# Kernel tuning notes

Measured on AMD Instinct MI355X. Metric: run time of the kernel, lower is better.

The kernel has to match this reference:

```python
import jax, jax.numpy as jnp
import numpy as np

B, C, H, W = 4, 64, 64, 64  # batch, channels (in==out), spatial


def _conv1x1(x, w, b):
    # x: (B, C, H, W), w: (O, C), b: (O,) -> (B, O, H, W)
    return jnp.einsum('bchw,oc->bohw', x, w) + b[None, :, None, None]


def setup_inputs() -> dict:
    key = jax.random.key(0)
    ks = jax.random.split(key, 7)
    s = 1.0 / np.sqrt(C)
    return {
        'x': jax.random.normal(ks[0], (B, C, H, W), dtype=jnp.float32),
        'Wq': jax.random.normal(ks[1], (C, C), dtype=jnp.float32) * s,
        'bq': jax.random.normal(ks[2], (C,), dtype=jnp.float32) * 0.01,
        'Wk': jax.random.normal(ks[3], (C, C), dtype=jnp.float32) * s,
        'bk': jax.random.normal(ks[4], (C,), dtype=jnp.float32) * 0.01,
        'Wv': jax.random.normal(ks[5], (C, C), dtype=jnp.float32) * s,
        'bv': jax.random.normal(ks[6], (C,), dtype=jnp.float32) * 0.01,
    }


def reference(x, Wq, bq, Wk, bk, Wv, bv):
    b, c, h, w = x.shape
    n = h * w  # number of spatial tokens
    q = _conv1x1(x, Wq, bq).reshape(b, c, n)  # (B, C, N)
    k = _conv1x1(x, Wk, bk).reshape(b, c, n)  # (B, C, N)
    v = _conv1x1(x, Wv, bv).reshape(b, c, n)  # (B, C, N)
    # attention[b, i, j] = softmax_j( q[:, i] . k[:, j] )  -- NOTE: no 1/sqrt(d) scaling, faithful to source
    scores = jnp.einsum('bci,bcj->bij', q, k)  # (B, N, N)
    attn = jax.nn.softmax(scores, axis=-1)
    # out = bmm(value, attention^T): out[b, c, i] = sum_j v[b, c, j] * attn[b, i, j]
    out = jnp.einsum('bcj,bij->bci', v, attn)
    return out.reshape(b, c, h, w)
```

## Files before the change

kernel.cpp:

```cpp
#include <hip/hip_runtime.h>
#include <hip/hip_bf16.h>


using f16    = _Float16;
using f16x8  = __attribute__((ext_vector_type(8))) f16;
using f32x16 = __attribute__((ext_vector_type(16))) float;
using i32x4  = __attribute__((ext_vector_type(4))) int;

static constexpr int NB = 4;
static constexpr int NC = 64;
static constexpr int NT = 4096;
static constexpr int KVB = 64;
static constexpr float LOG2E = 1.44269504088896f;

__device__ __forceinline__ float fexp2(float x) { return __builtin_amdgcn_exp2f(x); }
__device__ __forceinline__ unsigned int pkrtz(float a, float b) {
    return __builtin_bit_cast(unsigned int, __builtin_amdgcn_cvt_pkrtz(a, b));
}

__global__ __launch_bounds__(256) void qkv_proj(
    const float* __restrict__ x,
    const float* __restrict__ Wq, const float* __restrict__ bq,
    const float* __restrict__ Wk, const float* __restrict__ bk,
    const float* __restrict__ Wv, const float* __restrict__ bv,
    f16* __restrict__ qh, f16* __restrict__ kh, f16* __restrict__ vv)
{
    __shared__ f16 xT[64 * 64];
    __shared__ f16 wS[64 * 64];

    const int t  = threadIdx.x;
    const int p  = blockIdx.x >> 8;
    const int b  = (blockIdx.x >> 6) & 3;
    const int n0 = (blockIdx.x & 63) << 6;

    const float* Wp = (p == 0) ? Wq : (p == 1) ? Wk : Wv;
    const float* bp = (p == 0) ? bq : (p == 1) ? bk : bv;

    char* const xb = (char*)xT;
    char* const wb = (char*)wS;

    #pragma unroll
    for (int i = 0; i < 4; ++i) {
        const int idx = i * 256 + t;
        const int c = idx >> 4, n4 = (idx & 15) << 2;
        const float4 xv = *reinterpret_cast<const float4*>(
            x + ((size_t)(b * NC + c)) * NT + n0 + n4);
        const float xe[4] = {xv.x, xv.y, xv.z, xv.w};
        #pragma unroll
        for (int j = 0; j < 4; ++j) {
            const int n = n4 + j;
            *reinterpret_cast<f16*>(xb + n * 128 + ((c * 2) ^ ((n & 7) << 4))) =
                (f16)xe[j];
        }
        const int o = idx >> 4, c4 = (idx & 15) << 2;
        const float4 wv4 = *reinterpret_cast<const float4*>(Wp + o * 64 + c4);
        const uint2 pk = make_uint2(pkrtz(wv4.x, wv4.y), pkrtz(wv4.z, wv4.w));
        *reinterpret_cast<uint2*>(wb + o * 128 + ((c4 * 2) ^ ((o & 7) << 4))) = pk;
    }
    __syncthreads();

    const int lane = t & 63;
    const int wv   = t >> 6;
    const int l31  = lane & 31;
    const int hi   = lane >> 5;
    const int tr   = (wv & 1) << 5;
    const int tc   = (wv >> 1) << 5;

    f32x16 acc = {0,0,0,0,0,0,0,0,0,0,0,0,0,0,0,0};

    if (p < 2) {
        const int ra = tr + l31, rb = tc + l31;
        #pragma unroll
        for (int ks = 0; ks < 4; ++ks) {
            const int col = ks * 32 + hi * 16;
            const f16x8 a = *reinterpret_cast<const f16x8*>(
                xb + ra * 128 + (col ^ ((ra & 7) << 4)));
            const f16x8 bf = *reinterpret_cast<const f16x8*>(
                wb + rb * 128 + (col ^ ((rb & 7) << 4)));
            acc = __builtin_amdgcn_mfma_f32_32x32x16_f16(a, bf, acc, 0, 0, 0);
        }
        f16* hp = (p == 0) ? qh : kh;
        const float qs = (p == 0) ? LOG2E : 1.0f;
        const float bias = bp[tc + l31];
        #pragma unroll
        for (int r = 0; r < 16; ++r) {
            const int row = (r & 3) + 8 * (r >> 2) + 4 * hi;
            hp[((size_t)(b * NT + n0 + tr + row)) * NC + tc + l31] =
                (f16)((acc[r] + bias) * qs);
        }
    } else {
        const int ra = tr + l31, rb = tc + l31;
        #pragma unroll
        for (int ks = 0; ks < 4; ++ks) {
            const int col = ks * 32 + hi * 16;
            const f16x8 a = *reinterpret_cast<const f16x8*>(
                wb + ra * 128 + (col ^ ((ra & 7) << 4)));
            const f16x8 bf = *reinterpret_cast<const f16x8*>(
                xb + rb * 128 + (col ^ ((rb & 7) << 4)));
            acc = __builtin_amdgcn_mfma_f32_32x32x16_f16(a, bf, acc, 0, 0, 0);
        }
        #pragma unroll
        for (int r = 0; r < 16; ++r) {
            const int row = (r & 3) + 8 * (r >> 2) + 4 * hi;
            vv[((size_t)(b * NC + tr + row)) * NT + n0 + tc + l31] =
                (f16)(acc[r] + bp[tr + row]);
        }
    }
}

__global__ __launch_bounds__(256, 4) void attn_fused(
    const f16* __restrict__ qh, const f16* __restrict__ kh,
    const f16* __restrict__ vv, float* __restrict__ out,
    f16* __restrict__ pacc, float* __restrict__ pm,
    float* __restrict__ pl, int nTiles, int direct)
{
    __shared__ f16 khs[KVB * 64];
    __shared__ f16 vs_[64 * KVB];

    const int t    = threadIdx.x;
    const int lane = t & 63;
    const int wv   = t >> 6;
    const int l31  = lane & 31;
    const int hi   = lane >> 5;

    const int ngrp = (int)gridDim.x >> 5;
    int grp, i0;
    if ((ngrp & 7) == 0) {
        const int gpx  = ngrp >> 3;
        const int slot = (int)blockIdx.x >> 3;
        grp = ((int)blockIdx.x & 7) * gpx + (slot >> 5);
        i0  = (slot & 31) << 7;
    } else {
        grp = (int)blockIdx.x >> 5;
        i0  = ((int)blockIdx.x & 31) << 7;
    }
    const int s = grp >> 2;
    const int b = grp & 3;

    f16x8 qf[4];
    {
        const size_t qoff = ((size_t)(b * NT + i0 + wv * 32 + l31)) * NC + hi * 8;
        #pragma unroll
        for (int ks = 0; ks < 4; ++ks)
            qf[ks] = *reinterpret_cast<const f16x8*>(qh + qoff + ks * 16);
    }

    f32x16 acc0 = {0,0,0,0,0,0,0,0,0,0,0,0,0,0,0,0};
    f32x16 acc1 = {0,0,0,0,0,0,0,0,0,0,0,0,0,0,0,0};
    float m = -INFINITY, l = 0.f;

    const int row0 = t >> 3, c8 = (t & 7) << 3;
    const f16* kh_g = kh + (size_t)b * NT * NC;
    const f16* v_g  = vv + (size_t)b * NC * NT;

    char* const khsb = (char*)khs;
    char* const vsb  = (char*)vs_;
    const int kw0 = row0 * 128 + ((c8 << 1) ^ ((row0 & 7) << 4));
    const int kw1 = (row0 + 32) * 128 + ((c8 << 1) ^ (((row0 + 32) & 7) << 4));

    f16x8 stK0, stK1, stV0, stV1;
    auto stage_load = [&](int j0) {
        stK0 = *reinterpret_cast<const f16x8*>(kh_g + (size_t)(j0 + row0) * NC + c8);
        stK1 = *reinterpret_cast<const f16x8*>(kh_g + (size_t)(j0 + row0 + 32) * NC + c8);
        stV0 = *reinterpret_cast<const f16x8*>(v_g + (size_t)row0 * NT + j0 + c8);
        stV1 = *reinterpret_cast<const f16x8*>(v_g + (size_t)(row0 + 32) * NT + j0 + c8);
    };

    const int t0 = s * nTiles;
    stage_load(t0 * KVB);

    for (int k = 0; k < nTiles; ++k) {
        __syncthreads();
        *reinterpret_cast<f16x8*>(khsb + kw0) = stK0;
        *reinterpret_cast<f16x8*>(khsb + kw1) = stK1;
        *reinterpret_cast<f16x8*>(vsb + kw0)  = stV0;
        *reinterpret_cast<f16x8*>(vsb + kw1)  = stV1;
        __syncthreads();
        if (k + 1 < nTiles) stage_load((t0 + k + 1) * KVB);

        f32x16 sS0 = {0,0,0,0,0,0,0,0,0,0,0,0,0,0,0,0};
        f32x16 sS1 = {0,0,0,0,0,0,0,0,0,0,0,0,0,0,0,0};
        #pragma unroll
        for (int ks = 0; ks < 4; ++ks) {
            const int col = ks * 32 + hi * 16;
            const int r0 = l31;
            const f16x8 ak0 = *reinterpret_cast<const f16x8*>(
                khsb + r0 * 128 + (col ^ ((r0 & 7) << 4)));
            sS0 = __builtin_amdgcn_mfma_f32_32x32x16_f16(ak0, qf[ks], sS0, 0, 0, 0);
            const int r1 = 32 + l31;
            const f16x8 ak1 = *reinterpret_cast<const f16x8*>(
                khsb + r1 * 128 + (col ^ ((r1 & 7) << 4)));
            sS1 = __builtin_amdgcn_mfma_f32_32x32x16_f16(ak1, qf[ks], sS1, 0, 0, 0);
        }

        float mx[8];
        #pragma unroll
        for (int i = 0; i < 8; ++i)
            mx[i] = fmaxf(fmaxf(sS0[i], sS0[i + 8]), fmaxf(sS1[i], sS1[i + 8]));
        #pragma unroll
        for (int i = 0; i < 4; ++i) mx[i] = fmaxf(mx[i], mx[i + 4]);
        mx[0] = fmaxf(mx[0], mx[2]); mx[1] = fmaxf(mx[1], mx[3]);
        float mt = fmaxf(mx[0], mx[1]);
        mt = fmaxf(mt, __shfl_xor(mt, 32));
        const float mn = fmaxf(m, mt);

        float rs = 0.f;
        #pragma unroll
        for (int r = 0; r < 16; ++r) { sS0[r] = fexp2(sS0[r] - mn); rs += sS0[r]; }
        #pragma unroll
        for (int r = 0; r < 16; ++r) { sS1[r] = fexp2(sS1[r] - mn); rs += sS1[r]; }
        rs += __shfl_xor(rs, 32);

        if (__any(mt > m)) {
            const float sc = fexp2(m - mn);
            m = mn;
            l = l * sc + rs;
            #pragma unroll
            for (int r = 0; r < 16; ++r) { acc0[r] *= sc; acc1[r] *= sc; }
        } else {
            l += rs;
        }

        auto pv_sub = [&](const f32x16& sX, int kb) {
            unsigned int aw[4], bw[4];
            #pragma unroll
            for (int q4 = 0; q4 < 4; ++q4) {
                aw[q4] = pkrtz(sX[q4 * 4 + 0], sX[q4 * 4 + 1]);
                bw[q4] = pkrtz(sX[q4 * 4 + 2], sX[q4 * 4 + 3]);
            }
            #pragma unroll
            for (int ks = 0; ks < 2; ++ks) {
                const unsigned int ua = hi ? aw[2 * ks] : aw[2 * ks + 1];
                const unsigned int ub = hi ? bw[2 * ks] : bw[2 * ks + 1];
                const unsigned int sa = (unsigned int)__shfl_xor((int)ua, 32);
                const unsigned int sb = (unsigned int)__shfl_xor((int)ub, 32);
                const unsigned int w0 = hi ? sa : aw[2 * ks];
                const unsigned int w1 = hi ? sb : bw[2 * ks];
                const unsigned int w2 = hi ? aw[2 * ks + 1] : sa;
                const unsigned int w3 = hi ? bw[2 * ks + 1] : sb;
                const i32x4 wv4 = {(int)w0, (int)w1, (int)w2, (int)w3};
                const f16x8 bf = __builtin_bit_cast(f16x8, wv4);

                const int vcol = kb * 64 + ks * 32 + hi * 16;
                const int vrow0 = l31;
                const f16x8 av0 = *reinterpret_cast<const f16x8*>(
                    vsb + vrow0 * 128 + (vcol ^ ((vrow0 & 7) << 4)));
                acc0 = __builtin_amdgcn_mfma_f32_32x32x16_f16(av0, bf, acc0, 0, 0, 0);
                const int vrow1 = 32 + l31;
                const f16x8 av1 = *reinterpret_cast<const f16x8*>(
                    vsb + vrow1 * 128 + (vcol ^ ((vrow1 & 7) << 4)));
                acc1 = __builtin_amdgcn_mfma_f32_32x32x16_f16(av1, bf, acc1, 0, 0, 0);
            }
        };
        pv_sub(sS0, 0);
        pv_sub(sS1, 1);
    }

    const int q = i0 + wv * 32 + l31;
    const float linv = 1.f / l;
    if (direct) {
        const size_t ob = (size_t)b * NC * NT;
        #pragma unroll
        for (int r = 0; r < 16; ++r) {
            const int ch = (r & 3) + 8 * (r >> 2) + 4 * hi;
            out[ob + (size_t)ch * NT + q]        = acc0[r] * linv;
            out[ob + (size_t)(32 + ch) * NT + q] = acc1[r] * linv;
        }
    } else {
        const size_t pb = (size_t)(s * NB + b);
        #pragma unroll
        for (int r = 0; r < 16; ++r) {
            const int ch = (r & 3) + 8 * (r >> 2) + 4 * hi;
            pacc[(pb * NC + ch) * NT + q]      = (f16)(acc0[r] * linv);
            pacc[(pb * NC + 32 + ch) * NT + q] = (f16)(acc1[r] * linv);
        }
        if (hi == 0) {
            pm[pb * NT + q] = m;
            pl[pb * NT + q] = l;
        }
    }
}

__global__ __launch_bounds__(256) void merge_partials(
    const f16* __restrict__ pacc, const float* __restrict__ pm,
    const float* __restrict__ pl, float* __restrict__ out, int splits)
{
    const int t = threadIdx.x;
    const int i = ((blockIdx.x & 15) << 8) + t;
    const int c = (blockIdx.x >> 4) & 63;
    const int b = blockIdx.x >> 10;

    float M = -INFINITY;
    for (int s = 0; s < splits; ++s)
        M = fmaxf(M, pm[(size_t)(s * NB + b) * NT + i]);
    float L = 0.f, A = 0.f;
    for (int s = 0; s < splits; ++s) {
        const size_t pb = (size_t)(s * NB + b);
        const float wl = fexp2(pm[pb * NT + i] - M) * pl[pb * NT + i];
        L += wl;
        A += wl * (float)pacc[(pb * NC + c) * NT + i];
    }
    out[((size_t)b * NC + c) * NT + i] = A / L;
}

extern "C" void kernel_launch(void* const* d_in, const int* in_sizes, int n_in,
                              void* d_out, int out_size, void* d_ws, size_t ws_size,
                              hipStream_t stream)
{
    const float* x  = (const float*)d_in[0];
    const float* Wq = (const float*)d_in[1];
    const float* bq = (const float*)d_in[2];
    const float* Wk = (const float*)d_in[3];
    const float* bk = (const float*)d_in[4];
    const float* Wv = (const float*)d_in[5];
    const float* bv = (const float*)d_in[6];
    float* out = (float*)d_out;

    const size_t S = (size_t)NB * NT * NC;
    const size_t base_bytes = 6 * S;
    auto fits = [&](int sp) {
        return base_bytes + (size_t)sp * (2 * S + 2 * 4 * (size_t)NB * NT) <= ws_size;
    };
    const int splits = fits(8) ? 8 : fits(4) ? 4 : fits(2) ? 2 : fits(1) ? 1 : 0;

    f16* qh = (f16*)d_ws;
    f16* kh = qh + S;
    f16* vv = kh + S;

    qkv_proj<<<3 * NB * (NT / 64), 256, 0, stream>>>(x, Wq, bq, Wk, bk, Wv, bv,
                                                     qh, kh, vv);

    const int totTiles = NT / KVB;
    if (splits == 0) {
        attn_fused<<<NB * (NT / 128), 256, 0, stream>>>(
            qh, kh, vv, out, nullptr, nullptr, nullptr, totTiles, 1);
        return;
    }

    f16* pacc = vv + S;
    float* pm = (float*)(pacc + (size_t)splits * S);
    float* pl = pm + (size_t)splits * NB * NT;

    attn_fused<<<splits * NB * (NT / 128), 256, 0, stream>>>(
        qh, kh, vv, out, pacc, pm, pl, totTiles / splits, 0);
    merge_partials<<<NB * NC * (NT / 256), 256, 0, stream>>>(pacc, pm, pl, out, splits);
}
```

Before: 53.98 us.

## Double-buffer K/V via direct global-to-LDS loads, lazy max rescale, vectorize merge

The attention kernel now stages K and V tiles straight into LDS with global_load_lds into a double buffer, overlapping the next tile's load with current compute and dropping the register round-trip and one barrier per tile. The online softmax only rescales when the running max grows by more than 8 (log2 units), which skips most rescales but allows exp2 values up to 256 before fp16 packing. The merge kernel is vectorized so each thread handles 8 positions with float4/f16x8 loads, using far fewer blocks. Risks: the swizzle mapping must match the readers, there may be a missing wait on the asynchronous LDS loads, and the lazy threshold could cause fp16 precision loss or overflow.

```diff
diff --git a/kernel.cpp b/kernel.cpp
--- a/kernel.cpp
+++ b/kernel.cpp
@@ -16,6 +16,11 @@
 __device__ __forceinline__ float fexp2(float x) { return __builtin_amdgcn_exp2f(x); }
 __device__ __forceinline__ unsigned int pkrtz(float a, float b) {
     return __builtin_bit_cast(unsigned int, __builtin_amdgcn_cvt_pkrtz(a, b));
+}
+__device__ __forceinline__ void gload_lds16(const void* g, void* l) {
+    __builtin_amdgcn_global_load_lds(
+        (const __attribute__((address_space(1))) unsigned int*)g,
+        (__attribute__((address_space(3))) unsigned int*)l, 16, 0, 0);
 }
 
 __global__ __launch_bounds__(256) void qkv_proj(
@@ -114,8 +119,7 @@
     f16* __restrict__ pacc, float* __restrict__ pm,
     float* __restrict__ pl, int nTiles, int direct)
 {
-    __shared__ f16 khs[KVB * 64];
-    __shared__ f16 vs_[64 * KVB];
+    __shared__ f16 smem[2][2 * KVB * 64];
 
     const int t    = threadIdx.x;
     const int lane = t & 63;
@@ -149,34 +153,35 @@
     f32x16 acc1 = {0,0,0,0,0,0,0,0,0,0,0,0,0,0,0,0};
     float m = -INFINITY, l = 0.f;
 
-    const int row0 = t >> 3, c8 = (t & 7) << 3;
     const f16* kh_g = kh + (size_t)b * NT * NC;
     const f16* v_g  = vv + (size_t)b * NC * NT;
 
-    char* const khsb = (char*)khs;
-    char* const vsb  = (char*)vs_;
-    const int kw0 = row0 * 128 + ((c8 << 1) ^ ((row0 & 7) << 4));
-    const int kw1 = (row0 + 32) * 128 + ((c8 << 1) ^ (((row0 + 32) & 7) << 4));
-
-    f16x8 stK0, stK1, stV0, stV1;
-    auto stage_load = [&](int j0) {
-        stK0 = *reinterpret_cast<const f16x8*>(kh_g + (size_t)(j0 + row0) * NC + c8);
-        stK1 = *reinterpret_cast<const f16x8*>(kh_g + (size_t)(j0 + row0 + 32) * NC + c8);
-        stV0 = *reinterpret_cast<const f16x8*>(v_g + (size_t)row0 * NT + j0 + c8);
-        stV1 = *reinterpret_cast<const f16x8*>(v_g + (size_t)(row0 + 32) * NT + j0 + c8);
+    const int srow = (lane >> 3);
+    const int scol = (((lane & 7) ^ srow) << 3);
+    auto stage = [&](int j0, int buf) {
+        f16* const base = &smem[buf][0];
+        #pragma unroll
+        for (int i = 0; i < 4; ++i) {
+            const int idx = wv * 4 + i;
+            const int seg = idx & 7;
+            const int row = seg * 8 + srow;
+            f16* dst = base + (idx < 8 ? 0 : KVB * 64) + seg * 512 + (lane << 3);
+            const f16* src = (idx < 8)
+                ? kh_g + (size_t)(j0 + row) * NC + scol
+                : v_g + (size_t)row * NT + j0 + scol;
+            gload_lds16(src, dst);
+        }
     };
 
     const int t0 = s * nTiles;
-    stage_load(t0 * KVB);
+    stage(t0 * KVB, 0);
+    __syncthreads();
 
     for (int k = 0; k < nTiles; ++k) {
-        __syncthreads();
-        *reinterpret_cast<f16x8*>(khsb + kw0) = stK0;
-        *reinterpret_cast<f16x8*>(khsb + kw1) = stK1;
-        *reinterpret_cast<f16x8*>(vsb + kw0)  = stV0;
-        *reinterpret_cast<f16x8*>(vsb + kw1)  = stV1;
-        __syncthreads();
-        if (k + 1 < nTiles) stage_load((t0 + k + 1) * KVB);
+        if (k + 1 < nTiles) stage((t0 + k + 1) * KVB, (k + 1) & 1);
+
+        char* const khsb = (char*)&smem[k & 1][0];
+        char* const vsb  = khsb + KVB * 64 * 2;
 
         f32x16 sS0 = {0,0,0,0,0,0,0,0,0,0,0,0,0,0,0,0};
         f32x16 sS1 = {0,0,0,0,0,0,0,0,0,0,0,0,0,0,0,0};
@@ -202,7 +207,9 @@
         mx[0] = fmaxf(mx[0], mx[2]); mx[1] = fmaxf(mx[1], mx[3]);
         float mt = fmaxf(mx[0], mx[1]);
         mt = fmaxf(mt, __shfl_xor(mt, 32));
-        const float mn = fmaxf(m, mt);
+
+        const bool grow = __any(mt > m + 8.f);
+        const float mn = grow ? fmaxf(m, mt) : m;
 
         float rs = 0.f;
         #pragma unroll
@@ -211,7 +218,7 @@
         for (int r = 0; r < 16; ++r) { sS1[r] = fexp2(sS1[r] - mn); rs += sS1[r]; }
         rs += __shfl_xor(rs, 32);
 
-        if (__any(mt > m)) {
+        if (grow) {
             const float sc = fexp2(m - mn);
             m = mn;
             l = l * sc + rs;
@@ -254,6 +261,8 @@
         };
         pv_sub(sS0, 0);
         pv_sub(sS1, 1);
+
+        __syncthreads();
     }
 
     const int q = i0 + wv * 32 + l31;
@@ -285,22 +294,49 @@
     const f16* __restrict__ pacc, const float* __restrict__ pm,
     const float* __restrict__ pl, float* __restrict__ out, int splits)
 {
-    const int t = threadIdx.x;
-    const int i = ((blockIdx.x & 15) << 8) + t;
-    const int c = (blockIdx.x >> 4) & 63;
-    const int b = blockIdx.x >> 10;
-
-    float M = -INFINITY;
-    for (int s = 0; s < splits; ++s)
-        M = fmaxf(M, pm[(size_t)(s * NB + b) * NT + i]);
-    float L = 0.f, A = 0.f;
+    const int t  = threadIdx.x;
+    const int b  = blockIdx.x >> 7;
+    const int c  = (blockIdx.x >> 1) & 63;
+    const int i0 = ((((int)blockIdx.x & 1) << 8) + t) << 3;
+
+    float M[8];
+    #pragma unroll
+    for (int j = 0; j < 8; ++j) M[j] = -INFINITY;
+    for (int s = 0; s < splits; ++s) {
+        const float* pmb = pm + (size_t)(s * NB + b) * NT + i0;
+        const float4 a = *reinterpret_cast<const float4*>(pmb);
+        const float4 d = *reinterpret_cast<const float4*>(pmb + 4);
+        M[0] = fmaxf(M[0], a.x); M[1] = fmaxf(M[1], a.y);
+        M[2] = fmaxf(M[2], a.z); M[3] = fmaxf(M[3], a.w);
+        M[4] = fmaxf(M[4], d.x); M[5] = fmaxf(M[5], d.y);
+        M[6] = fmaxf(M[6], d.z); M[7] = fmaxf(M[7], d.w);
+    }
+    float L[8] = {0,0,0,0,0,0,0,0}, A[8] = {0,0,0,0,0,0,0,0};
     for (int s = 0; s < splits; ++s) {
         const size_t pb = (size_t)(s * NB + b);
-        const float wl = fexp2(pm[pb * NT + i] - M) * pl[pb * NT + i];
-        L += wl;
-        A += wl * (float)pacc[(pb * NC + c) * NT + i];
-    }
-    out[((size_t)b * NC + c) * NT + i] = A / L;
+        const float* pmb = pm + pb * NT + i0;
+        const float* plb = pl + pb * NT + i0;
+        const float4 m0 = *reinterpret_cast<const float4*>(pmb);
+        const float4 m1 = *reinterpret_cast<const float4*>(pmb + 4);
+        const float4 l0 = *reinterpret_cast<const float4*>(plb);
+        const float4 l1 = *reinterpret_cast<const float4*>(plb + 4);
+        const f16x8 pv = *reinterpret_cast<const f16x8*>(
+            pacc + (pb * NC + c) * NT + i0);
+        const float me[8] = {m0.x, m0.y, m0.z, m0.w, m1.x, m1.y, m1.z, m1.w};
+        const float le[8] = {l0.x, l0.y, l0.z, l0.w, l1.x, l1.y, l1.z, l1.w};
+        #pragma unroll
+        for (int j = 0; j < 8; ++j) {
+            const float wl = fexp2(me[j] - M[j]) * le[j];
+            L[j] += wl;
+            A[j] += wl * (float)pv[j];
+        }
+    }
+    float4 o0, o1;
+    o0.x = A[0] / L[0]; o0.y = A[1] / L[1]; o0.z = A[2] / L[2]; o0.w = A[3] / L[3];
+    o1.x = A[4] / L[4]; o1.y = A[5] / L[5]; o1.z = A[6] / L[6]; o1.w = A[7] / L[7];
+    float* ob = out + ((size_t)b * NC + c) * NT + i0;
+    *reinterpret_cast<float4*>(ob)     = o0;
+    *reinterpret_cast<float4*>(ob + 4) = o1;
 }
 
 extern "C" void kernel_launch(void* const* d_in, const int* in_sizes, int n_in,
@@ -343,5 +379,5 @@
 
     attn_fused<<<splits * NB * (NT / 128), 256, 0, stream>>>(
         qh, kh, vv, out, pacc, pm, pl, totTiles / splits, 0);
-    merge_partials<<<NB * NC * (NT / 256), 256, 0, stream>>>(pacc, pm, pl, out, splits);
-}
+    merge_partials<<<NB * 128, 256, 0, stream>>>(pacc, pm, pl, out, splits);
+}
```

Result: faster. 50.82 us (-5.9%).
